# Kernel tuning notes

Hardware: AMD Instinct MI355X
Metric: run time of the kernel (lower is better)

## Reference

```python
import jax, jax.numpy as jnp
import numpy as np

B, C, H, W = 32, 256, 8, 8
N = H * W                      # n_objects = 64
D_G_IN = 2 * C + 2             # pair concat + 2-dim relative position = 514
HG = 512                       # g hidden / output dim
HF = 512                       # f hidden dim
D_OUT = 256                    # f output dim


def _relative_grid_feat():
    # feat[p, q, 0] = oh(p) - oh(q); feat[p, q, 1] = ow(p) - ow(q); zero-centered globally
    idx = jnp.arange(N)
    oh, ow = idx // W, idx % W
    r0 = (oh[:, None] - oh[None, :]).astype(jnp.float32)
    r1 = (ow[:, None] - ow[None, :]).astype(jnp.float32)
    rel = jnp.stack([r0, r1], axis=-1)  # [N, N, 2]
    return rel - rel.mean()


def setup_inputs() -> dict:
    key = jax.random.key(0)
    ks = jax.random.split(key, 11)
    s = 0.02
    return {
        "x": jax.random.normal(ks[0], (B, C, H, W), dtype=jnp.float32),
        "g_W0": jax.random.normal(ks[1], (D_G_IN, HG), dtype=jnp.float32) * s,
        "g_b0": jnp.zeros((HG,), dtype=jnp.float32),
        "g_W1": jax.random.normal(ks[2], (HG, HG), dtype=jnp.float32) * s,
        "g_b1": jnp.zeros((HG,), dtype=jnp.float32),
        "g_W2": jax.random.normal(ks[3], (HG, HG), dtype=jnp.float32) * s,
        "g_b2": jnp.zeros((HG,), dtype=jnp.float32),
        "f_W0": jax.random.normal(ks[4], (HG, HF), dtype=jnp.float32) * s,
        "f_b0": jnp.zeros((HF,), dtype=jnp.float32),
        "f_W1": jax.random.normal(ks[5], (HF, D_OUT), dtype=jnp.float32) * s,
        "f_b1": jnp.zeros((D_OUT,), dtype=jnp.float32),
    }


def reference(x, g_W0, g_b0, g_W1, g_b1, g_W2, g_b2, f_W0, f_b0, f_W1, f_b1):
    relu = jax.nn.relu
    x_flat = x.reshape(B, C, N)                     # [B, C, N]
    xT = jnp.transpose(x_flat, (0, 2, 1))           # [B, N, C]
    # pair index k = p*N + q: xi takes object q (inner), xj takes object p (outer)
    xi = jnp.broadcast_to(xT[:, None, :, :], (B, N, N, C))
    xj = jnp.broadcast_to(xT[:, :, None, :], (B, N, N, C))
    rel = jnp.broadcast_to(_relative_grid_feat()[None], (B, N, N, 2))
    pair = jnp.concatenate([xi, xj, rel], axis=-1)  # [B, N, N, 2C+2]
    # g MLP (nonlinear=True -> activation on output too)
    h = relu(jnp.einsum('bpqd,dh->bpqh', pair, g_W0) + g_b0)
    h = relu(jnp.einsum('bpqh,hk->bpqk', h, g_W1) + g_b1)
    relations = relu(jnp.einsum('bpqh,hk->bpqk', h, g_W2) + g_b2)  # [B, N, N, HG]
    embedding = relations.sum(axis=(1, 2))          # sum over all pairs -> [B, HG]
    # f MLP (linear output)
    hf = relu(embedding @ f_W0 + f_b0)
    out = hf @ f_W1 + f_b1                          # [B, D_OUT]
    return out
```

## Files before the change

kernel.cpp:

```cpp
#include <hip/hip_runtime.h>


typedef short short8 __attribute__((ext_vector_type(8)));
typedef float f32x16 __attribute__((ext_vector_type(16)));

__device__ __forceinline__ unsigned short f2bf(float f) {
    unsigned u = __builtin_bit_cast(unsigned, f);
    u = (u + 0x7FFFu + ((u >> 16) & 1u)) >> 16;
    return (unsigned short)u;
}

__device__ __forceinline__ unsigned cvt_pk(float a, float b) {
    unsigned r;
    asm("v_cvt_pk_bf16_f32 %0, %1, %2" : "=v"(r) : "v"(a), "v"(b));
    return r;
}

__global__ __launch_bounds__(512) void pre_kernel(
    const float* __restrict__ x, const float* __restrict__ W0,
    const float* __restrict__ b0,
    const float* __restrict__ W1, const float* __restrict__ W2,
    float* __restrict__ Up, float* __restrict__ Vp,
    unsigned short* __restrict__ W1s, unsigned short* __restrict__ W2s,
    float* __restrict__ emb)
{
    __shared__ float xs[256 * 64];
    const int tid = threadIdx.x;

    if (blockIdx.x >= 256) {
        int gid = (blockIdx.x - 256) * 512 + tid;
        if (gid < 16384) emb[gid] = 0.f;
        int m = gid >> 15;
        int idx = gid & 32767;
        int col = idx & 511;
        int kg = idx >> 9;
        const float* W = m ? W2 : W1;
        unsigned short* O = m ? W2s : W1s;
        short8 v;
#pragma unroll
        for (int j = 0; j < 8; ++j)
            v[j] = (short)f2bf(W[(size_t)(kg * 8 + j) * 512 + col]);
        *(short8*)(O + (size_t)idx * 8) = v;
        return;
    }

    const int b = blockIdx.x >> 3, s = blockIdx.x & 7;
    const int g = tid >> 6;
    const int hL = tid & 63;
    const int h = s * 64 + hL;
    const int n0 = g * 8;

    {
        const float* xb = x + (size_t)b * 16384;
        for (int i = tid; i < 16384; i += 512) xs[i] = xb[i];
    }
    __syncthreads();

    float ua[8], va[8];
#pragma unroll
    for (int r = 0; r < 8; ++r) { ua[r] = 0.f; va[r] = 0.f; }

#pragma unroll 4
    for (int c = 0; c < 256; ++c) {
        float wa = W0[(size_t)c * 512 + h];
        float wb = W0[(size_t)(256 + c) * 512 + h];
        const float* xr = &xs[c * 64 + n0];
#pragma unroll
        for (int r = 0; r < 8; ++r) {
            float xv = xr[r];
            ua[r] += xv * wa;
            va[r] += xv * wb;
        }
    }
    const float w2a = W0[(size_t)512 * 512 + h];
    const float w2b = W0[(size_t)513 * 512 + h];
    const float bb = b0[h];
#pragma unroll
    for (int r = 0; r < 8; ++r) {
        int n = n0 + r;
        float fh = (float)(n >> 3), fw = (float)(n & 7);
        Up[((size_t)b * 64 + n) * 512 + h] = ua[r] - fh * w2a - fw * w2b;
        Vp[((size_t)b * 64 + n) * 512 + h] = va[r] + fh * w2a + fw * w2b + bb;
    }
}

__global__ __launch_bounds__(512, 2) void main_kernel(
    const float* __restrict__ Up, const float* __restrict__ Vp,
    const unsigned short* __restrict__ W1s, const unsigned short* __restrict__ W2s,
    const float* __restrict__ b1, const float* __restrict__ b2,
    float* __restrict__ emb)
{
    extern __shared__ __align__(16) unsigned char lds[];
    unsigned char* T0 = lds;
    unsigned char* T1 = lds + 65536;

    const int wg = ((blockIdx.x & 7) << 7) | (blockIdx.x >> 3);
    const int b = wg >> 5, pp = wg & 31;
    const int p0 = pp * 2, p1 = p0 + 1;

    const int tid = threadIdx.x;
    const int lane = tid & 63, wave = tid >> 6;
    const int l31 = lane & 31, lg = lane >> 5;
    const int swz = (l31 & 15) << 4;
    const int wcol = wave * 64;

    {
        const int cc = tid & 63;
        const int r0 = tid >> 6;
        float4 u0[8], u1[8];
#pragma unroll
        for (int it = 0; it < 8; ++it) {
            const float* ub = Up + ((size_t)(b * 64 + r0 + it * 8)) * 512 + cc * 8;
            u0[it] = *(const float4*)(ub);
            u1[it] = *(const float4*)(ub + 4);
        }
        const float* vA = Vp + ((size_t)(b * 64 + p0)) * 512 + cc * 8;
        const float* vB = Vp + ((size_t)(b * 64 + p1)) * 512 + cc * 8;
        float4 vA0 = *(const float4*)(vA), vA1 = *(const float4*)(vA + 4);
        float4 vB0 = *(const float4*)(vB), vB1 = *(const float4*)(vB + 4);
#pragma unroll
        for (int it = 0; it < 8; ++it) {
            int row = r0 + it * 8;
            int off = row * 1024 + ((cc * 16) ^ ((row & 15) << 4));
            uint4 w;
            w.x = cvt_pk(fmaxf(u0[it].x + vA0.x, 0.f), fmaxf(u0[it].y + vA0.y, 0.f));
            w.y = cvt_pk(fmaxf(u0[it].z + vA0.z, 0.f), fmaxf(u0[it].w + vA0.w, 0.f));
            w.z = cvt_pk(fmaxf(u1[it].x + vA1.x, 0.f), fmaxf(u1[it].y + vA1.y, 0.f));
            w.w = cvt_pk(fmaxf(u1[it].z + vA1.z, 0.f), fmaxf(u1[it].w + vA1.w, 0.f));
            *(uint4*)(&T0[off]) = w;
            w.x = cvt_pk(fmaxf(u0[it].x + vB0.x, 0.f), fmaxf(u0[it].y + vB0.y, 0.f));
            w.y = cvt_pk(fmaxf(u0[it].z + vB0.z, 0.f), fmaxf(u0[it].w + vB0.w, 0.f));
            w.z = cvt_pk(fmaxf(u1[it].x + vB1.x, 0.f), fmaxf(u1[it].y + vB1.y, 0.f));
            w.w = cvt_pk(fmaxf(u1[it].z + vB1.z, 0.f), fmaxf(u1[it].w + vB1.w, 0.f));
            *(uint4*)(&T1[off]) = w;
        }
    }
    __syncthreads();

    const int arow0 = l31 * 1024;
    const int arow1 = (l31 + 32) * 1024;

    f32x16 acc[2][2][2];
#pragma unroll
    for (int t = 0; t < 2; ++t)
#pragma unroll
        for (int i = 0; i < 2; ++i)
#pragma unroll
            for (int j = 0; j < 2; ++j) acc[t][i][j] = (f32x16)0.f;

    {
        const unsigned short* wb = W1s + ((size_t)(lg * 512 + wcol + l31)) * 8;
        short8 wc0[2], wc1[2];
        wc0[0] = *(const short8*)(wb);
        wc1[0] = *(const short8*)(wb + 256);
        wc0[1] = *(const short8*)(wb + 8192);
        wc1[1] = *(const short8*)(wb + 8192 + 256);
        __builtin_amdgcn_s_setprio(1);
#pragma unroll
        for (int ks = 0; ks < 32; ++ks) {
            const int par = ks & 1;
            short8 cw0 = wc0[par], cw1 = wc1[par];
            if (ks < 30) {
                const unsigned short* np = wb + (size_t)(ks + 2) * 8192;
                wc0[par] = *(const short8*)(np);
                wc1[par] = *(const short8*)(np + 256);
            }
            int achunk = (ks * 32 + lg * 16) ^ swz;
            short8 a00 = *(const short8*)(&T0[arow0 + achunk]);
            short8 a01 = *(const short8*)(&T0[arow1 + achunk]);
            short8 a10 = *(const short8*)(&T1[arow0 + achunk]);
            short8 a11 = *(const short8*)(&T1[arow1 + achunk]);
            acc[0][0][0] = __builtin_amdgcn_mfma_f32_32x32x16_bf16(cw0, a00, acc[0][0][0], 0, 0, 0);
            acc[0][1][0] = __builtin_amdgcn_mfma_f32_32x32x16_bf16(cw1, a00, acc[0][1][0], 0, 0, 0);
            acc[0][0][1] = __builtin_amdgcn_mfma_f32_32x32x16_bf16(cw0, a01, acc[0][0][1], 0, 0, 0);
            acc[0][1][1] = __builtin_amdgcn_mfma_f32_32x32x16_bf16(cw1, a01, acc[0][1][1], 0, 0, 0);
            acc[1][0][0] = __builtin_amdgcn_mfma_f32_32x32x16_bf16(cw0, a10, acc[1][0][0], 0, 0, 0);
            acc[1][1][0] = __builtin_amdgcn_mfma_f32_32x32x16_bf16(cw1, a10, acc[1][1][0], 0, 0, 0);
            acc[1][0][1] = __builtin_amdgcn_mfma_f32_32x32x16_bf16(cw0, a11, acc[1][0][1], 0, 0, 0);
            acc[1][1][1] = __builtin_amdgcn_mfma_f32_32x32x16_bf16(cw1, a11, acc[1][1][1], 0, 0, 0);
        }
        __builtin_amdgcn_s_setprio(0);
    }
    __syncthreads();

    {
#pragma unroll
        for (int hf = 0; hf < 2; ++hf) {
#pragma unroll
            for (int g = 0; g < 4; ++g) {
                int h = wcol + hf * 32 + g * 8 + 4 * lg;
                float4 bb = *(const float4*)(b1 + h);
#pragma unroll
                for (int t = 0; t < 2; ++t) {
#pragma unroll
                    for (int qf = 0; qf < 2; ++qf) {
                        int q = qf * 32 + l31;
                        float a0 = fmaxf(acc[t][hf][qf][g * 4 + 0] + bb.x, 0.f);
                        float a1 = fmaxf(acc[t][hf][qf][g * 4 + 1] + bb.y, 0.f);
                        float a2 = fmaxf(acc[t][hf][qf][g * 4 + 2] + bb.z, 0.f);
                        float a3 = fmaxf(acc[t][hf][qf][g * 4 + 3] + bb.w, 0.f);
                        uint2 pk;
                        pk.x = cvt_pk(a0, a1);
                        pk.y = cvt_pk(a2, a3);
                        int off = q * 1024 + ((h * 2) ^ ((q & 15) << 4));
                        unsigned char* Tt = t ? T1 : T0;
                        *(uint2*)(&Tt[off]) = pk;
                    }
                }
            }
        }
    }
    __syncthreads();

    f32x16 acc2[2][2][2];
#pragma unroll
    for (int t = 0; t < 2; ++t)
#pragma unroll
        for (int i = 0; i < 2; ++i)
#pragma unroll
            for (int j = 0; j < 2; ++j) acc2[t][i][j] = (f32x16)0.f;

    {
        const unsigned short* wb = W2s + ((size_t)(lg * 512 + wcol + l31)) * 8;
        short8 wc0[2], wc1[2];
        wc0[0] = *(const short8*)(wb);
        wc1[0] = *(const short8*)(wb + 256);
        wc0[1] = *(const short8*)(wb + 8192);
        wc1[1] = *(const short8*)(wb + 8192 + 256);
        __builtin_amdgcn_s_setprio(1);
#pragma unroll
        for (int ks = 0; ks < 32; ++ks) {
            const int par = ks & 1;
            short8 cw0 = wc0[par], cw1 = wc1[par];
            if (ks < 30) {
                const unsigned short* np = wb + (size_t)(ks + 2) * 8192;
                wc0[par] = *(const short8*)(np);
                wc1[par] = *(const short8*)(np + 256);
            }
            int achunk = (ks * 32 + lg * 16) ^ swz;
            short8 a00 = *(const short8*)(&T0[arow0 + achunk]);
            short8 a01 = *(const short8*)(&T0[arow1 + achunk]);
            short8 a10 = *(const short8*)(&T1[arow0 + achunk]);
            short8 a11 = *(const short8*)(&T1[arow1 + achunk]);
            acc2[0][0][0] = __builtin_amdgcn_mfma_f32_32x32x16_bf16(a00, cw0, acc2[0][0][0], 0, 0, 0);
            acc2[0][1][0] = __builtin_amdgcn_mfma_f32_32x32x16_bf16(a01, cw0, acc2[0][1][0], 0, 0, 0);
            acc2[0][0][1] = __builtin_amdgcn_mfma_f32_32x32x16_bf16(a00, cw1, acc2[0][0][1], 0, 0, 0);
            acc2[0][1][1] = __builtin_amdgcn_mfma_f32_32x32x16_bf16(a01, cw1, acc2[0][1][1], 0, 0, 0);
            acc2[1][0][0] = __builtin_amdgcn_mfma_f32_32x32x16_bf16(a10, cw0, acc2[1][0][0], 0, 0, 0);
            acc2[1][1][0] = __builtin_amdgcn_mfma_f32_32x32x16_bf16(a11, cw0, acc2[1][1][0], 0, 0, 0);
            acc2[1][0][1] = __builtin_amdgcn_mfma_f32_32x32x16_bf16(a10, cw1, acc2[1][0][1], 0, 0, 0);
            acc2[1][1][1] = __builtin_amdgcn_mfma_f32_32x32x16_bf16(a11, cw1, acc2[1][1][1], 0, 0, 0);
        }
        __builtin_amdgcn_s_setprio(0);
    }

    {
        float s[2];
#pragma unroll
        for (int cf = 0; cf < 2; ++cf) {
            int col = wcol + cf * 32 + l31;
            float bias = b2[col];
            float tt = 0.f;
#pragma unroll
            for (int t = 0; t < 2; ++t)
#pragma unroll
                for (int rf = 0; rf < 2; ++rf)
#pragma unroll
                    for (int reg = 0; reg < 16; ++reg)
                        tt += fmaxf(acc2[t][rf][cf][reg] + bias, 0.f);
            tt += __shfl_xor(tt, 32);
            s[cf] = tt;
        }
        if (lane < 32) {
            unsafeAtomicAdd(&emb[b * 512 + wcol + lane], s[0]);
            unsafeAtomicAdd(&emb[b * 512 + wcol + 32 + lane], s[1]);
        }
    }
}

__global__ __launch_bounds__(256) void f0_kernel(
    const float* __restrict__ emb, const float* __restrict__ fW0,
    const float* __restrict__ fb0, float* __restrict__ hs)
{
    __shared__ float es[512];
    __shared__ float red[256];
    const int b = blockIdx.x >> 3, s = blockIdx.x & 7;
    const int t = threadIdx.x;
    const int colL = t & 63, cg = t >> 6;
    es[t] = emb[b * 512 + t];
    es[t + 256] = emb[b * 512 + 256 + t];
    __syncthreads();
    const int col = s * 64 + colL;
    float a = 0.f;
    const int c0 = cg * 128;
#pragma unroll 4
    for (int c = c0; c < c0 + 128; ++c)
        a += es[c] * fW0[(size_t)c * 512 + col];
    red[t] = a;
    __syncthreads();
    if (t < 64) {
        float r = red[t] + red[t + 64] + red[t + 128] + red[t + 192] + fb0[col];
        hs[b * 512 + col] = fmaxf(r, 0.f);
    }
}

__global__ __launch_bounds__(256) void f1_kernel(
    const float* __restrict__ hs, const float* __restrict__ fW1,
    const float* __restrict__ fb1, float* __restrict__ out)
{
    __shared__ float es[512];
    __shared__ float red[256];
    const int b = blockIdx.x >> 2, s = blockIdx.x & 3;
    const int t = threadIdx.x;
    const int colL = t & 63, cg = t >> 6;
    es[t] = hs[b * 512 + t];
    es[t + 256] = hs[b * 512 + 256 + t];
    __syncthreads();
    const int col = s * 64 + colL;
    float a = 0.f;
    const int c0 = cg * 128;
#pragma unroll 4
    for (int c = c0; c < c0 + 128; ++c)
        a += es[c] * fW1[(size_t)c * 256 + col];
    red[t] = a;
    __syncthreads();
    if (t < 64) {
        out[b * 256 + col] = red[t] + red[t + 64] + red[t + 128] + red[t + 192] + fb1[col];
    }
}

extern "C" void kernel_launch(void* const* d_in, const int* in_sizes, int n_in,
                              void* d_out, int out_size, void* d_ws, size_t ws_size,
                              hipStream_t stream)
{
    const float* x   = (const float*)d_in[0];
    const float* gW0 = (const float*)d_in[1];
    const float* gb0 = (const float*)d_in[2];
    const float* gW1 = (const float*)d_in[3];
    const float* gb1 = (const float*)d_in[4];
    const float* gW2 = (const float*)d_in[5];
    const float* gb2 = (const float*)d_in[6];
    const float* fW0 = (const float*)d_in[7];
    const float* fb0 = (const float*)d_in[8];
    const float* fW1 = (const float*)d_in[9];
    const float* fb1 = (const float*)d_in[10];
    float* out = (float*)d_out;

    char* ws = (char*)d_ws;
    float* Up           = (float*)(ws);
    float* Vp           = (float*)(ws + (4 << 20));
    unsigned short* W1s = (unsigned short*)(ws + (8 << 20));
    unsigned short* W2s = (unsigned short*)(ws + (8 << 20) + (512 << 10));
    float* emb          = (float*)(ws + (9 << 20));
    float* hs           = (float*)(ws + (9 << 20) + (64 << 10));

    pre_kernel<<<384, 512, 0, stream>>>(x, gW0, gb0, gW1, gW2, Up, Vp, W1s, W2s, emb);
    main_kernel<<<1024, 512, 131072, stream>>>(Up, Vp, W1s, W2s, gb1, gb2, emb);
    f0_kernel<<<256, 256, 0, stream>>>(emb, fW0, fb0, hs);
    f1_kernel<<<128, 256, 0, stream>>>(hs, fW1, fb1, out);
}
```

Measured before the change: 171.5 us.

## Repartition waves so each handles one pair tile and 128 output columns

Each wave previously computed 64 hidden columns for both p-tiles (T0 and T1), loading two weight fragments and four A fragments per k-step. Now wave parity picks the tile and each wave covers 128 columns, loading four weight fragments and two A fragments per step. This halves LDS reads of activations per wave but doubles global/L2 weight fragment loads per wave and register use for weight prefetch. Each wave also writes back only into its own tile.

```diff
diff --git a/kernel.cpp b/kernel.cpp
--- a/kernel.cpp
+++ b/kernel.cpp
@@ -102,7 +102,9 @@
     const int lane = tid & 63, wave = tid >> 6;
     const int l31 = lane & 31, lg = lane >> 5;
     const int swz = (l31 & 15) << 4;
-    const int wcol = wave * 64;
+    const int t = wave & 1;
+    const int wcol = (wave >> 1) << 7;
+    unsigned char* T = t ? T1 : T0;
 
     {
         const int cc = tid & 63;
@@ -140,44 +142,46 @@
     const int arow0 = l31 * 1024;
     const int arow1 = (l31 + 32) * 1024;
 
-    f32x16 acc[2][2][2];
-#pragma unroll
-    for (int t = 0; t < 2; ++t)
-#pragma unroll
-        for (int i = 0; i < 2; ++i)
-#pragma unroll
-            for (int j = 0; j < 2; ++j) acc[t][i][j] = (f32x16)0.f;
+    f32x16 acc[4][2];
+#pragma unroll
+    for (int i = 0; i < 4; ++i)
+#pragma unroll
+        for (int j = 0; j < 2; ++j) acc[i][j] = (f32x16)0.f;
 
     {
         const unsigned short* wb = W1s + ((size_t)(lg * 512 + wcol + l31)) * 8;
-        short8 wc0[2], wc1[2];
+        short8 wc0[2], wc1[2], wc2[2], wc3[2];
         wc0[0] = *(const short8*)(wb);
         wc1[0] = *(const short8*)(wb + 256);
+        wc2[0] = *(const short8*)(wb + 512);
+        wc3[0] = *(const short8*)(wb + 768);
         wc0[1] = *(const short8*)(wb + 8192);
         wc1[1] = *(const short8*)(wb + 8192 + 256);
+        wc2[1] = *(const short8*)(wb + 8192 + 512);
+        wc3[1] = *(const short8*)(wb + 8192 + 768);
         __builtin_amdgcn_s_setprio(1);
 #pragma unroll
         for (int ks = 0; ks < 32; ++ks) {
             const int par = ks & 1;
-            short8 cw0 = wc0[par], cw1 = wc1[par];
+            short8 cw0 = wc0[par], cw1 = wc1[par], cw2 = wc2[par], cw3 = wc3[par];
             if (ks < 30) {
                 const unsigned short* np = wb + (size_t)(ks + 2) * 8192;
                 wc0[par] = *(const short8*)(np);
                 wc1[par] = *(const short8*)(np + 256);
+                wc2[par] = *(const short8*)(np + 512);
+                wc3[par] = *(const short8*)(np + 768);
             }
             int achunk = (ks * 32 + lg * 16) ^ swz;
-            short8 a00 = *(const short8*)(&T0[arow0 + achunk]);
-            short8 a01 = *(const short8*)(&T0[arow1 + achunk]);
-            short8 a10 = *(const short8*)(&T1[arow0 + achunk]);
-            short8 a11 = *(const short8*)(&T1[arow1 + achunk]);
-            acc[0][0][0] = __builtin_amdgcn_mfma_f32_32x32x16_bf16(cw0, a00, acc[0][0][0], 0, 0, 0);
-            acc[0][1][0] = __builtin_amdgcn_mfma_f32_32x32x16_bf16(cw1, a00, acc[0][1][0], 0, 0, 0);
-            acc[0][0][1] = __builtin_amdgcn_mfma_f32_32x32x16_bf16(cw0, a01, acc[0][0][1], 0, 0, 0);
-            acc[0][1][1] = __builtin_amdgcn_mfma_f32_32x32x16_bf16(cw1, a01, acc[0][1][1], 0, 0, 0);
-            acc[1][0][0] = __builtin_amdgcn_mfma_f32_32x32x16_bf16(cw0, a10, acc[1][0][0], 0, 0, 0);
-            acc[1][1][0] = __builtin_amdgcn_mfma_f32_32x32x16_bf16(cw1, a10, acc[1][1][0], 0, 0, 0);
-            acc[1][0][1] = __builtin_amdgcn_mfma_f32_32x32x16_bf16(cw0, a11, acc[1][0][1], 0, 0, 0);
-            acc[1][1][1] = __builtin_amdgcn_mfma_f32_32x32x16_bf16(cw1, a11, acc[1][1][1], 0, 0, 0);
+            short8 a0 = *(const short8*)(&T[arow0 + achunk]);
+            short8 a1 = *(const short8*)(&T[arow1 + achunk]);
+            acc[0][0] = __builtin_amdgcn_mfma_f32_32x32x16_bf16(cw0, a0, acc[0][0], 0, 0, 0);
+            acc[1][0] = __builtin_amdgcn_mfma_f32_32x32x16_bf16(cw1, a0, acc[1][0], 0, 0, 0);
+            acc[2][0] = __builtin_amdgcn_mfma_f32_32x32x16_bf16(cw2, a0, acc[2][0], 0, 0, 0);
+            acc[3][0] = __builtin_amdgcn_mfma_f32_32x32x16_bf16(cw3, a0, acc[3][0], 0, 0, 0);
+            acc[0][1] = __builtin_amdgcn_mfma_f32_32x32x16_bf16(cw0, a1, acc[0][1], 0, 0, 0);
+            acc[1][1] = __builtin_amdgcn_mfma_f32_32x32x16_bf16(cw1, a1, acc[1][1], 0, 0, 0);
+            acc[2][1] = __builtin_amdgcn_mfma_f32_32x32x16_bf16(cw2, a1, acc[2][1], 0, 0, 0);
+            acc[3][1] = __builtin_amdgcn_mfma_f32_32x32x16_bf16(cw3, a1, acc[3][1], 0, 0, 0);
         }
         __builtin_amdgcn_s_setprio(0);
     }
@@ -185,95 +189,87 @@
 
     {
 #pragma unroll
-        for (int hf = 0; hf < 2; ++hf) {
+        for (int hf = 0; hf < 4; ++hf) {
 #pragma unroll
             for (int g = 0; g < 4; ++g) {
                 int h = wcol + hf * 32 + g * 8 + 4 * lg;
                 float4 bb = *(const float4*)(b1 + h);
 #pragma unroll
-                for (int t = 0; t < 2; ++t) {
-#pragma unroll
-                    for (int qf = 0; qf < 2; ++qf) {
-                        int q = qf * 32 + l31;
-                        float a0 = fmaxf(acc[t][hf][qf][g * 4 + 0] + bb.x, 0.f);
-                        float a1 = fmaxf(acc[t][hf][qf][g * 4 + 1] + bb.y, 0.f);
-                        float a2 = fmaxf(acc[t][hf][qf][g * 4 + 2] + bb.z, 0.f);
-                        float a3 = fmaxf(acc[t][hf][qf][g * 4 + 3] + bb.w, 0.f);
-                        uint2 pk;
-                        pk.x = cvt_pk(a0, a1);
-                        pk.y = cvt_pk(a2, a3);
-                        int off = q * 1024 + ((h * 2) ^ ((q & 15) << 4));
-                        unsigned char* Tt = t ? T1 : T0;
-                        *(uint2*)(&Tt[off]) = pk;
-                    }
+                for (int qf = 0; qf < 2; ++qf) {
+                    int q = qf * 32 + l31;
+                    float a0 = fmaxf(acc[hf][qf][g * 4 + 0] + bb.x, 0.f);
+                    float a1 = fmaxf(acc[hf][qf][g * 4 + 1] + bb.y, 0.f);
+                    float a2 = fmaxf(acc[hf][qf][g * 4 + 2] + bb.z, 0.f);
+                    float a3 = fmaxf(acc[hf][qf][g * 4 + 3] + bb.w, 0.f);
+                    uint2 pk;
+                    pk.x = cvt_pk(a0, a1);
+                    pk.y = cvt_pk(a2, a3);
+                    int off = q * 1024 + ((h * 2) ^ ((q & 15) << 4));
+                    *(uint2*)(&T[off]) = pk;
                 }
             }
         }
     }
     __syncthreads();
 
-    f32x16 acc2[2][2][2];
-#pragma unroll
-    for (int t = 0; t < 2; ++t)
-#pragma unroll
-        for (int i = 0; i < 2; ++i)
-#pragma unroll
-            for (int j = 0; j < 2; ++j) acc2[t][i][j] = (f32x16)0.f;
+    f32x16 acc2[2][4];
+#pragma unroll
+    for (int i = 0; i < 2; ++i)
+#pragma unroll
+        for (int j = 0; j < 4; ++j) acc2[i][j] = (f32x16)0.f;
 
     {
         const unsigned short* wb = W2s + ((size_t)(lg * 512 + wcol + l31)) * 8;
-        short8 wc0[2], wc1[2];
+        short8 wc0[2], wc1[2], wc2[2], wc3[2];
         wc0[0] = *(const short8*)(wb);
         wc1[0] = *(const short8*)(wb + 256);
+        wc2[0] = *(const short8*)(wb + 512);
+        wc3[0] = *(const short8*)(wb + 768);
         wc0[1] = *(const short8*)(wb + 8192);
         wc1[1] = *(const short8*)(wb + 8192 + 256);
+        wc2[1] = *(const short8*)(wb + 8192 + 512);
+        wc3[1] = *(const short8*)(wb + 8192 + 768);
         __builtin_amdgcn_s_setprio(1);
 #pragma unroll
         for (int ks = 0; ks < 32; ++ks) {
             const int par = ks & 1;
-            short8 cw0 = wc0[par], cw1 = wc1[par];
+            short8 cw0 = wc0[par], cw1 = wc1[par], cw2 = wc2[par], cw3 = wc3[par];
             if (ks < 30) {
                 const unsigned short* np = wb + (size_t)(ks + 2) * 8192;
                 wc0[par] = *(const short8*)(np);
                 wc1[par] = *(const short8*)(np + 256);
+                wc2[par] = *(const short8*)(np + 512);
+                wc3[par] = *(const short8*)(np + 768);
             }
             int achunk = (ks * 32 + lg * 16) ^ swz;
-            short8 a00 = *(const short8*)(&T0[arow0 + achunk]);
-            short8 a01 = *(const short8*)(&T0[arow1 + achunk]);
-            short8 a10 = *(const short8*)(&T1[arow0 + achunk]);
-            short8 a11 = *(const short8*)(&T1[arow1 + achunk]);
-            acc2[0][0][0] = __builtin_amdgcn_mfma_f32_32x32x16_bf16(a00, cw0, acc2[0][0][0], 0, 0, 0);
-            acc2[0][1][0] = __builtin_amdgcn_mfma_f32_32x32x16_bf16(a01, cw0, acc2[0][1][0], 0, 0, 0);
-            acc2[0][0][1] = __builtin_amdgcn_mfma_f32_32x32x16_bf16(a00, cw1, acc2[0][0][1], 0, 0, 0);
-            acc2[0][1][1] = __builtin_amdgcn_mfma_f32_32x32x16_bf16(a01, cw1, acc2[0][1][1], 0, 0, 0);
-            acc2[1][0][0] = __builtin_amdgcn_mfma_f32_32x32x16_bf16(a10, cw0, acc2[1][0][0], 0, 0, 0);
-            acc2[1][1][0] = __builtin_amdgcn_mfma_f32_32x32x16_bf16(a11, cw0, acc2[1][1][0], 0, 0, 0);
-            acc2[1][0][1] = __builtin_amdgcn_mfma_f32_32x32x16_bf16(a10, cw1, acc2[1][0][1], 0, 0, 0);
-            acc2[1][1][1] = __builtin_amdgcn_mfma_f32_32x32x16_bf16(a11, cw1, acc2[1][1][1], 0, 0, 0);
+            short8 a0 = *(const short8*)(&T[arow0 + achunk]);
+            short8 a1 = *(const short8*)(&T[arow1 + achunk]);
+            acc2[0][0] = __builtin_amdgcn_mfma_f32_32x32x16_bf16(a0, cw0, acc2[0][0], 0, 0, 0);
+            acc2[1][0] = __builtin_amdgcn_mfma_f32_32x32x16_bf16(a1, cw0, acc2[1][0], 0, 0, 0);
+            acc2[0][1] = __builtin_amdgcn_mfma_f32_32x32x16_bf16(a0, cw1, acc2[0][1], 0, 0, 0);
+            acc2[1][1] = __builtin_amdgcn_mfma_f32_32x32x16_bf16(a1, cw1, acc2[1][1], 0, 0, 0);
+            acc2[0][2] = __builtin_amdgcn_mfma_f32_32x32x16_bf16(a0, cw2, acc2[0][2], 0, 0, 0);
+            acc2[1][2] = __builtin_amdgcn_mfma_f32_32x32x16_bf16(a1, cw2, acc2[1][2], 0, 0, 0);
+            acc2[0][3] = __builtin_amdgcn_mfma_f32_32x32x16_bf16(a0, cw3, acc2[0][3], 0, 0, 0);
+            acc2[1][3] = __builtin_amdgcn_mfma_f32_32x32x16_bf16(a1, cw3, acc2[1][3], 0, 0, 0);
         }
         __builtin_amdgcn_s_setprio(0);
     }
 
     {
-        float s[2];
-#pragma unroll
-        for (int cf = 0; cf < 2; ++cf) {
+#pragma unroll
+        for (int cf = 0; cf < 4; ++cf) {
             int col = wcol + cf * 32 + l31;
             float bias = b2[col];
             float tt = 0.f;
 #pragma unroll
-            for (int t = 0; t < 2; ++t)
-#pragma unroll
-                for (int rf = 0; rf < 2; ++rf)
-#pragma unroll
-                    for (int reg = 0; reg < 16; ++reg)
-                        tt += fmaxf(acc2[t][rf][cf][reg] + bias, 0.f);
+            for (int qf = 0; qf < 2; ++qf)
+#pragma unroll
+                for (int reg = 0; reg < 16; ++reg)
+                    tt += fmaxf(acc2[qf][cf][reg] + bias, 0.f);
             tt += __shfl_xor(tt, 32);
-            s[cf] = tt;
-        }
-        if (lane < 32) {
-            unsafeAtomicAdd(&emb[b * 512 + wcol + lane], s[0]);
-            unsafeAtomicAdd(&emb[b * 512 + wcol + 32 + lane], s[1]);
+            if (lane < 32)
+                unsafeAtomicAdd(&emb[b * 512 + col], tt);
         }
     }
 }
```

After: 191.7 us. +11.8%, slower.
